# Kernel tuning notes

Hardware: AMD Instinct MI355X
Metric: run time of the kernel (lower is better)

Reference implementation:

```python
import jax, jax.numpy as jnp
import numpy as np
import math

D_MODEL = 512
DK = D_MODEL // 4      # per-head dim = 128
DH = D_MODEL // 8      # half-head dim = 64
BS, QL, SL = 4, 2048, 2048


def setup_inputs() -> dict:
    key = jax.random.key(0)
    ks = jax.random.split(key, 16)
    h = D_MODEL // 2
    inp = {
        "q": jax.random.normal(ks[0], (2, BS, QL, h), jnp.float32),
        "k": jax.random.normal(ks[1], (2, BS, SL, h), jnp.float32),
        "v": jax.random.normal(ks[2], (2, BS, SL, h), jnp.float32),
        "q_spa_embed": jax.random.normal(ks[3], (BS, 1, DK, DK), jnp.float32) * 0.1,
        "kv_spa_embed": jax.random.normal(ks[4], (BS, SL, DK, DK), jnp.float32) * 0.1,
        "attention_bias": jax.random.normal(ks[5], (BS, SL), jnp.float32),
        "mask": jax.random.randint(ks[6], (BS, SL), 0, 2, jnp.int32),
        # Linear weights stored [in, out] (torch Linear(in,out).weight.T)
        "W_qa": jax.random.normal(ks[7], (h, h // 2), jnp.float32) / math.sqrt(h),
        "W_qb": jax.random.normal(ks[8], (h, h // 2), jnp.float32) / math.sqrt(h),
        "W_ka": jax.random.normal(ks[9], (h, h // 2), jnp.float32) / math.sqrt(h),
        "W_kb": jax.random.normal(ks[10], (h, h // 2), jnp.float32) / math.sqrt(h),
        "W_va": jax.random.normal(ks[11], (h, h // 2), jnp.float32) / math.sqrt(h),
        "W_vb": jax.random.normal(ks[12], (h, h // 2), jnp.float32) / math.sqrt(h),
        "W_oa": jax.random.normal(ks[13], (h, h), jnp.float32) / math.sqrt(h),
        "W_ob": jax.random.normal(ks[14], (h, h), jnp.float32) / math.sqrt(h),
    }
    return inp


def _make_heads(xa, xb):
    # xa, xb: [bs, L, d_model//4] -> [bs, 4, L, dk] with head pattern
    # (a0,b0),(a1,b0),(a0,b1),(a1,b1)
    bs, L, _ = xa.shape
    xa = xa.reshape(bs, L, 2, DH)
    xb = xb.reshape(bs, L, 2, DH)
    xa = jnp.tile(xa, (1, 1, 2, 1))            # [bs,L,4,DH]
    xb = jnp.repeat(xb, 2, axis=2)             # [bs,L,4,DH]
    return jnp.concatenate([xa, xb], axis=-1).transpose(0, 2, 1, 3)  # [bs,4,L,DK]


def reference(q, k, v, q_spa_embed, kv_spa_embed, attention_bias, mask,
              W_qa, W_qb, W_ka, W_kb, W_va, W_vb, W_oa, W_ob):
    bs, ql = q.shape[1], q.shape[2]
    sl = k.shape[2]
    qh = _make_heads(q[0] @ W_qa, q[1] @ W_qb)   # [bs,4,ql,DK]
    kh = _make_heads(k[0] @ W_ka, k[1] @ W_kb)   # [bs,4,sl,DK]
    vh = _make_heads(v[0] @ W_va, v[1] @ W_vb)   # [bs,4,sl,DK]

    # per-token spatial rotation (seq_len == kv_spa_embed.shape[1] branch)
    qh = jnp.einsum('bij,bhqj->bhqi', q_spa_embed[:, 0], qh)
    kh = jnp.einsum('bsij,bhsj->bhsi', kv_spa_embed, kh)

    scores = jnp.einsum('bhqd,bhsd->bhqs', qh, kh) / math.sqrt(D_MODEL // 4)
    scores = scores + mask.astype(scores.dtype)[:, None, None, :] * (-1e9)
    attn = jax.nn.softmax(scores - attention_bias[:, None, None, :], axis=-1)
    # dropout: identity (eval mode)
    out = jnp.einsum('bhqs,bhsd->bhqd', attn, vh)          # [bs,4,ql,DK]

    out = out.reshape(bs, 4, ql, 2, DH)
    oa = out[:, :, :, 0].transpose(0, 2, 1, 3).reshape(bs, ql, -1) @ W_oa
    ob = out[:, :, :, 1].transpose(0, 2, 1, 3).reshape(bs, ql, -1) @ W_ob
    return jnp.stack([oa, ob], axis=0), attn
```

## Files before the change

### kernel.cpp

```cpp
#include <hip/hip_runtime.h>
#include <math.h>

#define QL 2048
#define SL 2048
#define BS 4
#define NH 4
#define FSZ ((size_t)BS * QL * 128)
#define OSZ ((size_t)2 * BS * QL * 256)

typedef short bf16x8 __attribute__((ext_vector_type(8)));
typedef float f32x4 __attribute__((ext_vector_type(4)));

__device__ __forceinline__ short to_bf16_rne(float x) {
    unsigned u = __float_as_uint(x);
    unsigned r = u + 0x7fffu + ((u >> 16) & 1u);
    return (short)(r >> 16);
}

__device__ __forceinline__ void split8(const float* x, bf16x8& hi, bf16x8& lo) {
    #pragma unroll
    for (int j = 0; j < 8; j++) {
        short hh = to_bf16_rne(x[j]);
        float hf = __uint_as_float(((unsigned)(unsigned short)hh) << 16);
        hi[j] = hh;
        lo[j] = to_bf16_rne(x[j] - hf);
    }
}

__global__ __launch_bounds__(256) void proj_mfma_kernel(
    const float* __restrict__ q, const float* __restrict__ k, const float* __restrict__ v,
    const float* __restrict__ Wqa, const float* __restrict__ Wqb,
    const float* __restrict__ Wka, const float* __restrict__ Wkb,
    const float* __restrict__ Wva, const float* __restrict__ Wvb,
    float* __restrict__ ws)
{
    int id = blockIdx.y;
    const float* X; const float* W;
    const size_t HALF = (size_t)BS * QL * 256;
    switch (id) {
      case 0: X = q;        W = Wqa; break;
      case 1: X = q + HALF; W = Wqb; break;
      case 2: X = k;        W = Wka; break;
      case 3: X = k + HALF; W = Wkb; break;
      case 4: X = v;        W = Wva; break;
      default:X = v + HALF; W = Wvb; break;
    }
    float* Y = ws + (size_t)id * FSZ;
    int m0 = blockIdx.x * 128;

    __shared__ short lA[128 * 64];
    __shared__ short lB[128 * 64];

    int t = threadIdx.x;
    int srow = t >> 1, shalf = t & 1;
    int l = t & 63, w = t >> 6;
    int wr = w >> 1, wc = w & 1;
    int lr = l & 15, kb = l >> 4;

    f32x4 acc[4][4] = {};

    for (int kc = 0; kc < 256; kc += 32) {
        {
            const float* srcA = X + (size_t)(m0 + srow) * 256 + kc + shalf * 16;
            float xa[16];
            #pragma unroll
            for (int j = 0; j < 4; j++)
                *(float4*)&xa[j * 4] = *(const float4*)(srcA + j * 4);
            bf16x8 h0, l0, h1, l1;
            split8(&xa[0], h0, l0);
            split8(&xa[8], h1, l1);
            int base = srow * 64, r7 = srow & 7;
            *(bf16x8*)&lA[base + (((4 * shalf + 0) ^ r7) * 8)] = h0;
            *(bf16x8*)&lA[base + (((4 * shalf + 1) ^ r7) * 8)] = l0;
            *(bf16x8*)&lA[base + (((4 * shalf + 2) ^ r7) * 8)] = h1;
            *(bf16x8*)&lA[base + (((4 * shalf + 3) ^ r7) * 8)] = l1;
        }
        {
            int ncol = srow;
            float xb[16];
            #pragma unroll
            for (int j = 0; j < 16; j++)
                xb[j] = W[(size_t)(kc + shalf * 16 + j) * 128 + ncol];
            bf16x8 h0, l0, h1, l1;
            split8(&xb[0], h0, l0);
            split8(&xb[8], h1, l1);
            int base = ncol * 64, r7 = ncol & 7;
            *(bf16x8*)&lB[base + (((4 * shalf + 0) ^ r7) * 8)] = h0;
            *(bf16x8*)&lB[base + (((4 * shalf + 1) ^ r7) * 8)] = l0;
            *(bf16x8*)&lB[base + (((4 * shalf + 2) ^ r7) * 8)] = h1;
            *(bf16x8*)&lB[base + (((4 * shalf + 3) ^ r7) * 8)] = l1;
        }
        __syncthreads();

        bf16x8 ah[4], al[4], bhv[4], blv[4];
        #pragma unroll
        for (int m = 0; m < 4; m++) {
            int r = wr * 64 + m * 16 + lr;
            int r7 = r & 7, base = r * 64;
            ah[m] = *(bf16x8*)&lA[base + (((2 * kb + 0) ^ r7) * 8)];
            al[m] = *(bf16x8*)&lA[base + (((2 * kb + 1) ^ r7) * 8)];
        }
        #pragma unroll
        for (int n = 0; n < 4; n++) {
            int r = wc * 64 + n * 16 + lr;
            int r7 = r & 7, base = r * 64;
            bhv[n] = *(bf16x8*)&lB[base + (((2 * kb + 0) ^ r7) * 8)];
            blv[n] = *(bf16x8*)&lB[base + (((2 * kb + 1) ^ r7) * 8)];
        }
        #pragma unroll
        for (int m = 0; m < 4; m++) {
            #pragma unroll
            for (int n = 0; n < 4; n++) {
                acc[m][n] = __builtin_amdgcn_mfma_f32_16x16x32_bf16(ah[m], bhv[n], acc[m][n], 0, 0, 0);
                acc[m][n] = __builtin_amdgcn_mfma_f32_16x16x32_bf16(ah[m], blv[n], acc[m][n], 0, 0, 0);
                acc[m][n] = __builtin_amdgcn_mfma_f32_16x16x32_bf16(al[m], bhv[n], acc[m][n], 0, 0, 0);
            }
        }
        __syncthreads();
    }

    #pragma unroll
    for (int n = 0; n < 4; n++) {
        int gcol = wc * 64 + n * 16 + lr;
        #pragma unroll
        for (int m = 0; m < 4; m++) {
            int grow = m0 + wr * 64 + m * 16 + kb * 4;
            float* dst = Y + (size_t)grow * 128 + gcol;
            f32x4 c = acc[m][n];
            dst[0 * 128] = c[0];
            dst[1 * 128] = c[1];
            dst[2 * 128] = c[2];
            dst[3 * 128] = c[3];
        }
    }
}

__global__ __launch_bounds__(256) void rot_split_kernel(
    const float* __restrict__ qa, const float* __restrict__ qb,
    const float* __restrict__ ka, const float* __restrict__ kb,
    const float* __restrict__ qse, const float* __restrict__ kvse,
    short* __restrict__ qrotS, short* __restrict__ krotS)
{
    int tkn = blockIdx.x;
    int b = blockIdx.y;
    int z = blockIdx.z;
    const float* ha = z ? ka : qa;
    const float* hb = z ? kb : qb;
    const float* E = z ? (kvse + (size_t)(b * SL + tkn) * 16384)
                       : (qse + (size_t)b * 16384);
    short* rotS = z ? krotS : qrotS;

    __shared__ float hv[4][128];
    __shared__ float outl[4][128];
    int tid = threadIdx.x;
    size_t tok = (size_t)(b * QL + tkn) * 128;
    for (int idx = tid; idx < 512; idx += 256) {
        int h = idx >> 7, d = idx & 127;
        float val = (d < 64) ? ha[tok + (h & 1) * 64 + d]
                             : hb[tok + (h >> 1) * 64 + (d - 64)];
        hv[h][d] = val;
    }
    __syncthreads();
    int w = tid >> 6, lane = tid & 63;
    int half = lane >> 5, l5 = lane & 31;
    for (int it = 0; it < 16; ++it) {
        int i = w * 32 + it * 2 + half;
        float4 e = *(const float4*)(E + (size_t)i * 128 + l5 * 4);
        float acc[4];
        #pragma unroll
        for (int h = 0; h < 4; h++) {
            float4 x = *(const float4*)&hv[h][l5 * 4];
            acc[h] = e.x * x.x + e.y * x.y + e.z * x.z + e.w * x.w;
        }
        #pragma unroll
        for (int off = 1; off < 32; off <<= 1) {
            #pragma unroll
            for (int h = 0; h < 4; h++) acc[h] += __shfl_xor(acc[h], off);
        }
        if (l5 < 4) outl[l5][i] = acc[l5];
    }
    __syncthreads();
    if (tid < 128) {
        int h    = tid >> 5;
        int kcid = (tid >> 3) & 3;
        int s    = tid & 7;
        int shalf = s >> 2;
        int isLo  = s & 1;
        int jbase = ((s >> 1) & 1) * 8;
        int dbase = kcid * 32 + shalf * 16 + jbase;
        bf16x8 outv;
        #pragma unroll
        for (int j = 0; j < 8; j++) {
            float x = outl[h][dbase + j];
            short hh = to_bf16_rne(x);
            if (isLo) {
                float hf = __uint_as_float(((unsigned)(unsigned short)hh) << 16);
                outv[j] = to_bf16_rne(x - hf);
            } else {
                outv[j] = hh;
            }
        }
        int bh = b * NH + h;
        int row = tkn & 127;
        size_t base = ((((size_t)bh * 16 + (tkn >> 7)) * 4 + kcid) * 128 + row) * 64;
        *(bf16x8*)&rotS[base + (size_t)((s ^ (row & 7)) * 8)] = outv;
    }
}

__global__ __launch_bounds__(256) void score_mfma_kernel(
    const short* __restrict__ qrotS, const short* __restrict__ krotS,
    const float* __restrict__ bias, const int* __restrict__ mask,
    float* __restrict__ attn, float* __restrict__ stats)
{
    __shared__ short lA[128 * 64];
    __shared__ short lB[128 * 64];
    __shared__ float redM[128][2];
    __shared__ float redS[128][2];

    int bid = blockIdx.x;
    int wg = (bid & 7) * 512 + (bid >> 3);
    int bh = wg >> 8;
    int qt = (wg >> 4) & 15, st = wg & 15;
    int q0 = qt * 128, s0 = st * 128;
    int b = bh >> 2;

    int t = threadIdx.x;
    int l = t & 63, w = t >> 6;
    int wr = w >> 1, wc = w & 1;
    int lr = l & 15, kb = l >> 4;

    const short* Abase = qrotS + (((size_t)bh * 16 + qt) * 4) * 8192;
    const short* Bbase = krotS + (((size_t)bh * 16 + st) * 4) * 8192;

    f32x4 acc[4][4] = {};

    for (int kcid = 0; kcid < 4; kcid++) {
        {
            const bf16x8* srcA = (const bf16x8*)(Abase + (size_t)kcid * 8192) + t * 4;
            const bf16x8* srcB = (const bf16x8*)(Bbase + (size_t)kcid * 8192) + t * 4;
            bf16x8 a0 = srcA[0], a1 = srcA[1], a2 = srcA[2], a3 = srcA[3];
            bf16x8 b0 = srcB[0], b1 = srcB[1], b2 = srcB[2], b3 = srcB[3];
            bf16x8* dA = (bf16x8*)lA + t * 4;
            bf16x8* dB = (bf16x8*)lB + t * 4;
            dA[0] = a0; dA[1] = a1; dA[2] = a2; dA[3] = a3;
            dB[0] = b0; dB[1] = b1; dB[2] = b2; dB[3] = b3;
        }
        __syncthreads();

        bf16x8 ah[4], al[4], bhv[4], blv[4];
        #pragma unroll
        for (int m = 0; m < 4; m++) {
            int r = wr * 64 + m * 16 + lr;
            int r7 = r & 7, base = r * 64;
            ah[m] = *(bf16x8*)&lA[base + (((2 * kb + 0) ^ r7) * 8)];
            al[m] = *(bf16x8*)&lA[base + (((2 * kb + 1) ^ r7) * 8)];
        }
        #pragma unroll
        for (int n = 0; n < 4; n++) {
            int r = wc * 64 + n * 16 + lr;
            int r7 = r & 7, base = r * 64;
            bhv[n] = *(bf16x8*)&lB[base + (((2 * kb + 0) ^ r7) * 8)];
            blv[n] = *(bf16x8*)&lB[base + (((2 * kb + 1) ^ r7) * 8)];
        }
        #pragma unroll
        for (int m = 0; m < 4; m++) {
            #pragma unroll
            for (int n = 0; n < 4; n++) {
                acc[m][n] = __builtin_amdgcn_mfma_f32_16x16x32_bf16(ah[m], bhv[n], acc[m][n], 0, 0, 0);
                acc[m][n] = __builtin_amdgcn_mfma_f32_16x16x32_bf16(ah[m], blv[n], acc[m][n], 0, 0, 0);
                acc[m][n] = __builtin_amdgcn_mfma_f32_16x16x32_bf16(al[m], bhv[n], acc[m][n], 0, 0, 0);
            }
        }
        __syncthreads();
    }

    const float scale = 0.08838834764831845f;
    #pragma unroll
    for (int n = 0; n < 4; n++) {
        int gs = s0 + wc * 64 + n * 16 + lr;
        float adj = -1e9f * (float)mask[b * SL + gs] - bias[b * SL + gs];
        #pragma unroll
        for (int m = 0; m < 4; m++) {
            int gq = q0 + wr * 64 + m * 16 + kb * 4;
            float* dst = attn + ((size_t)bh * QL + gq) * SL + gs;
            f32x4 c = acc[m][n];
            c[0] = c[0] * scale + adj;
            c[1] = c[1] * scale + adj;
            c[2] = c[2] * scale + adj;
            c[3] = c[3] * scale + adj;
            acc[m][n] = c;
            dst[0 * SL] = c[0];
            dst[1 * SL] = c[1];
            dst[2 * SL] = c[2];
            dst[3 * SL] = c[3];
        }
    }

    #pragma unroll
    for (int m = 0; m < 4; m++) {
        #pragma unroll
        for (int i = 0; i < 4; i++) {
            float rm = fmaxf(fmaxf(acc[m][0][i], acc[m][1][i]),
                             fmaxf(acc[m][2][i], acc[m][3][i]));
            rm = fmaxf(rm, __shfl_xor(rm, 1));
            rm = fmaxf(rm, __shfl_xor(rm, 2));
            rm = fmaxf(rm, __shfl_xor(rm, 4));
            rm = fmaxf(rm, __shfl_xor(rm, 8));
            if (lr == 0) redM[wr * 64 + m * 16 + kb * 4 + i][wc] = rm;
        }
    }
    __syncthreads();
    #pragma unroll
    for (int m = 0; m < 4; m++) {
        #pragma unroll
        for (int i = 0; i < 4; i++) {
            int row = wr * 64 + m * 16 + kb * 4 + i;
            float mt = fmaxf(redM[row][0], redM[row][1]);
            float es = __expf(acc[m][0][i] - mt) + __expf(acc[m][1][i] - mt)
                     + __expf(acc[m][2][i] - mt) + __expf(acc[m][3][i] - mt);
            es += __shfl_xor(es, 1);
            es += __shfl_xor(es, 2);
            es += __shfl_xor(es, 4);
            es += __shfl_xor(es, 8);
            if (lr == 0) redS[row][wc] = es;
        }
    }
    __syncthreads();
    if (t < 128) {
        float mt = fmaxf(redM[t][0], redM[t][1]);
        float es = redS[t][0] + redS[t][1];
        size_t r = (size_t)bh * QL + q0 + t;
        stats[(r * 16 + st) * 2 + 0] = mt;
        stats[(r * 16 + st) * 2 + 1] = es;
    }
}

__global__ __launch_bounds__(256) void sreduce_kernel(
    const float* __restrict__ stats,
    float* __restrict__ rowm, float* __restrict__ rowinv)
{
    int r = blockIdx.x * 256 + threadIdx.x;
    const float* src = stats + (size_t)r * 32;
    float4 p[8];
    #pragma unroll
    for (int j = 0; j < 8; j++) p[j] = *(const float4*)(src + j * 4);
    float m = -INFINITY;
    #pragma unroll
    for (int j = 0; j < 8; j++) { m = fmaxf(m, p[j].x); m = fmaxf(m, p[j].z); }
    float s = 0.f;
    #pragma unroll
    for (int j = 0; j < 8; j++) {
        s += p[j].y * __expf(p[j].x - m);
        s += p[j].w * __expf(p[j].z - m);
    }
    rowm[r] = m;
    rowinv[r] = 1.0f / s;
}

__global__ __launch_bounds__(256) void vtrans_kernel(
    const float* __restrict__ va, const float* __restrict__ vb,
    short* __restrict__ vT)
{
    int sblk = blockIdx.x;
    int bh = blockIdx.y;
    int b = bh >> 2, h = bh & 3;
    int hao = (h & 1) * 64, hbo = (h >> 1) * 64;
    __shared__ float vt[32][132];
    int t = threadIdx.x;
    for (int f = t; f < 1024; f += 256) {
        int s = f >> 5, c4 = (f & 31) * 4;
        size_t tok = (size_t)(b * SL + sblk * 32 + s) * 128;
        float4 vv = (c4 < 64) ? *(const float4*)(va + tok + hao + c4)
                              : *(const float4*)(vb + tok + hbo + (c4 - 64));
        *(float4*)&vt[s][c4] = vv;
    }
    __syncthreads();
    int d = t >> 1, shalf = t & 1;
    bf16x8 hi[2], lo[2];
    #pragma unroll
    for (int kb2 = 0; kb2 < 2; kb2++) {
        int kb = shalf * 2 + kb2;
        #pragma unroll
        for (int j = 0; j < 8; j++) {
            float x = vt[kb * 8 + j][d];
            short hh = to_bf16_rne(x);
            float hf = __uint_as_float(((unsigned)(unsigned short)hh) << 16);
            hi[kb2][j] = hh;
            lo[kb2][j] = to_bf16_rne(x - hf);
        }
    }
    size_t base = (((size_t)bh * 64 + sblk) * 128 + d) * 64;
    int d7 = d & 7;
    *(bf16x8*)&vT[base + (size_t)(((2 * (shalf * 2 + 0) + 0) ^ d7) * 8)] = hi[0];
    *(bf16x8*)&vT[base + (size_t)(((2 * (shalf * 2 + 0) + 1) ^ d7) * 8)] = lo[0];
    *(bf16x8*)&vT[base + (size_t)(((2 * (shalf * 2 + 1) + 0) ^ d7) * 8)] = hi[1];
    *(bf16x8*)&vT[base + (size_t)(((2 * (shalf * 2 + 1) + 1) ^ d7) * 8)] = lo[1];
}

__global__ __launch_bounds__(256) void pv_fused_kernel(
    float* __restrict__ attn, const short* __restrict__ vT,
    const float* __restrict__ rowm, const float* __restrict__ rowinv,
    float* __restrict__ outh)
{
    __shared__ short lA[128 * 64];
    __shared__ short lB[128 * 64];

    int bid = blockIdx.x;
    int wg = (bid & 7) * 32 + (bid >> 3);
    int bh = wg >> 4, qt = wg & 15;
    int q0 = qt * 128;

    float* Ag = attn + ((size_t)bh * QL + q0) * SL;
    const short* Bg = vT + (size_t)bh * 64 * 8192;

    int t = threadIdx.x;
    int srow = t >> 1, shalf = t & 1;
    int l = t & 63, w = t >> 6;
    int wr = w >> 1, wc = w & 1;
    int lr = l & 15, kb = l >> 4;

    float rm  = rowm[(size_t)bh * QL + q0 + srow];
    float riv = rowinv[(size_t)bh * QL + q0 + srow];

    f32x4 acc[4][4] = {};

    for (int sblk = 0; sblk < 64; sblk++) {
        {
            float* src = Ag + (size_t)srow * SL + sblk * 32 + shalf * 16;
            float x[16];
            #pragma unroll
            for (int j = 0; j < 4; j++)
                *(float4*)&x[j * 4] = *(const float4*)(src + j * 4);
            #pragma unroll
            for (int j = 0; j < 16; j++)
                x[j] = __expf(x[j] - rm) * riv;
            #pragma unroll
            for (int j = 0; j < 4; j++)
                *(float4*)(src + j * 4) = *(float4*)&x[j * 4];
            bf16x8 h0, l0, h1, l1;
            split8(&x[0], h0, l0);
            split8(&x[8], h1, l1);
            int base = srow * 64, r7 = srow & 7;
            *(bf16x8*)&lA[base + (((4 * shalf + 0) ^ r7) * 8)] = h0;
            *(bf16x8*)&lA[base + (((4 * shalf + 1) ^ r7) * 8)] = l0;
            *(bf16x8*)&lA[base + (((4 * shalf + 2) ^ r7) * 8)] = h1;
            *(bf16x8*)&lA[base + (((4 * shalf + 3) ^ r7) * 8)] = l1;
        }
        {
            const bf16x8* src = (const bf16x8*)(Bg + (size_t)sblk * 8192) + t * 4;
            bf16x8 v0 = src[0], v1 = src[1], v2 = src[2], v3 = src[3];
            bf16x8* dst = (bf16x8*)lB + t * 4;
            dst[0] = v0; dst[1] = v1; dst[2] = v2; dst[3] = v3;
        }
        __syncthreads();

        bf16x8 ah[4], al[4], bhv[4], blv[4];
        #pragma unroll
        for (int m = 0; m < 4; m++) {
            int r = wr * 64 + m * 16 + lr;
            int r7 = r & 7, base = r * 64;
            ah[m] = *(bf16x8*)&lA[base + (((2 * kb + 0) ^ r7) * 8)];
            al[m] = *(bf16x8*)&lA[base + (((2 * kb + 1) ^ r7) * 8)];
        }
        #pragma unroll
        for (int n = 0; n < 4; n++) {
            int r = wc * 64 + n * 16 + lr;
            int r7 = r & 7, base = r * 64;
            bhv[n] = *(bf16x8*)&lB[base + (((2 * kb + 0) ^ r7) * 8)];
            blv[n] = *(bf16x8*)&lB[base + (((2 * kb + 1) ^ r7) * 8)];
        }
        #pragma unroll
        for (int m = 0; m < 4; m++) {
            #pragma unroll
            for (int n = 0; n < 4; n++) {
                acc[m][n] = __builtin_amdgcn_mfma_f32_16x16x32_bf16(ah[m], bhv[n], acc[m][n], 0, 0, 0);
                acc[m][n] = __builtin_amdgcn_mfma_f32_16x16x32_bf16(ah[m], blv[n], acc[m][n], 0, 0, 0);
                acc[m][n] = __builtin_amdgcn_mfma_f32_16x16x32_bf16(al[m], bhv[n], acc[m][n], 0, 0, 0);
            }
        }
        __syncthreads();
    }

    #pragma unroll
    for (int n = 0; n < 4; n++) {
        int gd = wc * 64 + n * 16 + lr;
        #pragma unroll
        for (int m = 0; m < 4; m++) {
            int gq = q0 + wr * 64 + m * 16 + kb * 4;
            float* dst = outh + ((size_t)bh * QL + gq) * 128 + gd;
            f32x4 c = acc[m][n];
            dst[0 * 128] = c[0];
            dst[1 * 128] = c[1];
            dst[2 * 128] = c[2];
            dst[3 * 128] = c[3];
        }
    }
}

__global__ __launch_bounds__(256) void oproj_mfma_kernel(
    const float* __restrict__ outh, const float* __restrict__ Woa, const float* __restrict__ Wob,
    float* __restrict__ opart)
{
    int bt = blockIdx.x;
    int b = bt >> 4, tt = bt & 15;
    int t0 = tt * 128;
    int n0 = blockIdx.y * 128;
    int sel = blockIdx.z >> 1;
    int ks  = blockIdx.z & 1;
    const float* W = sel ? Wob : Woa;
    int doff = sel ? 64 : 0;

    __shared__ short lA[128 * 64];
    __shared__ short lB[128 * 64];

    int t = threadIdx.x;
    int srow = t >> 1, shalf = t & 1;
    int l = t & 63, w = t >> 6;
    int wr = w >> 1, wc = w & 1;
    int lr = l & 15, kb = l >> 4;

    f32x4 acc[4][4] = {};

    for (int kc = ks * 128; kc < ks * 128 + 128; kc += 32) {
        {
            int k0 = kc + shalf * 16;
            int h = k0 >> 6, d0 = k0 & 63;
            const float* srcA = outh + ((size_t)(b * NH + h) * QL + t0 + srow) * 128 + doff + d0;
            float xa[16];
            #pragma unroll
            for (int j = 0; j < 4; j++)
                *(float4*)&xa[j * 4] = *(const float4*)(srcA + j * 4);
            bf16x8 h0, l0, h1, l1;
            split8(&xa[0], h0, l0);
            split8(&xa[8], h1, l1);
            int base = srow * 64, r7 = srow & 7;
            *(bf16x8*)&lA[base + (((4 * shalf + 0) ^ r7) * 8)] = h0;
            *(bf16x8*)&lA[base + (((4 * shalf + 1) ^ r7) * 8)] = l0;
            *(bf16x8*)&lA[base + (((4 * shalf + 2) ^ r7) * 8)] = h1;
            *(bf16x8*)&lA[base + (((4 * shalf + 3) ^ r7) * 8)] = l1;
        }
        {
            int ncol = srow;
            float xb[16];
            #pragma unroll
            for (int j = 0; j < 16; j++)
                xb[j] = W[(size_t)(kc + shalf * 16 + j) * 256 + n0 + ncol];
            bf16x8 h0, l0, h1, l1;
            split8(&xb[0], h0, l0);
            split8(&xb[8], h1, l1);
            int base = ncol * 64, r7 = ncol & 7;
            *(bf16x8*)&lB[base + (((4 * shalf + 0) ^ r7) * 8)] = h0;
            *(bf16x8*)&lB[base + (((4 * shalf + 1) ^ r7) * 8)] = l0;
            *(bf16x8*)&lB[base + (((4 * shalf + 2) ^ r7) * 8)] = h1;
            *(bf16x8*)&lB[base + (((4 * shalf + 3) ^ r7) * 8)] = l1;
        }
        __syncthreads();

        bf16x8 ah[4], al[4], bhv[4], blv[4];
        #pragma unroll
        for (int m = 0; m < 4; m++) {
            int r = wr * 64 + m * 16 + lr;
            int r7 = r & 7, base = r * 64;
            ah[m] = *(bf16x8*)&lA[base + (((2 * kb + 0) ^ r7) * 8)];
            al[m] = *(bf16x8*)&lA[base + (((2 * kb + 1) ^ r7) * 8)];
        }
        #pragma unroll
        for (int n = 0; n < 4; n++) {
            int r = wc * 64 + n * 16 + lr;
            int r7 = r & 7, base = r * 64;
            bhv[n] = *(bf16x8*)&lB[base + (((2 * kb + 0) ^ r7) * 8)];
            blv[n] = *(bf16x8*)&lB[base + (((2 * kb + 1) ^ r7) * 8)];
        }
        #pragma unroll
        for (int m = 0; m < 4; m++) {
            #pragma unroll
            for (int n = 0; n < 4; n++) {
                acc[m][n] = __builtin_amdgcn_mfma_f32_16x16x32_bf16(ah[m], bhv[n], acc[m][n], 0, 0, 0);
                acc[m][n] = __builtin_amdgcn_mfma_f32_16x16x32_bf16(ah[m], blv[n], acc[m][n], 0, 0, 0);
                acc[m][n] = __builtin_amdgcn_mfma_f32_16x16x32_bf16(al[m], bhv[n], acc[m][n], 0, 0, 0);
            }
        }
        __syncthreads();
    }

    float* dstbase = opart + (size_t)ks * OSZ;
    #pragma unroll
    for (int n = 0; n < 4; n++) {
        int gcol = n0 + wc * 64 + n * 16 + lr;
        #pragma unroll
        for (int m = 0; m < 4; m++) {
            int grow = t0 + wr * 64 + m * 16 + kb * 4;
            float* dst = dstbase + ((size_t)((sel * BS + b) * QL) + grow) * 256 + gcol;
            f32x4 c = acc[m][n];
            dst[0 * 256] = c[0];
            dst[1 * 256] = c[1];
            dst[2 * 256] = c[2];
            dst[3 * 256] = c[3];
        }
    }
}

__global__ __launch_bounds__(256) void oadd_kernel(
    const float* __restrict__ opart, float* __restrict__ outp)
{
    size_t i = ((size_t)blockIdx.x * 256 + threadIdx.x) * 4;
    float4 a = *(const float4*)(opart + i);
    float4 b = *(const float4*)(opart + OSZ + i);
    float4 o = make_float4(a.x + b.x, a.y + b.y, a.z + b.z, a.w + b.w);
    *(float4*)(outp + i) = o;
}

extern "C" void kernel_launch(void* const* d_in, const int* in_sizes, int n_in,
                              void* d_out, int out_size, void* d_ws, size_t ws_size,
                              hipStream_t stream)
{
    const float* q    = (const float*)d_in[0];
    const float* k    = (const float*)d_in[1];
    const float* v    = (const float*)d_in[2];
    const float* qse  = (const float*)d_in[3];
    const float* kvse = (const float*)d_in[4];
    const float* bias = (const float*)d_in[5];
    const int*   mask = (const int*)d_in[6];
    const float* Wqa  = (const float*)d_in[7];
    const float* Wqb  = (const float*)d_in[8];
    const float* Wka  = (const float*)d_in[9];
    const float* Wkb  = (const float*)d_in[10];
    const float* Wva  = (const float*)d_in[11];
    const float* Wvb  = (const float*)d_in[12];
    const float* Woa  = (const float*)d_in[13];
    const float* Wob  = (const float*)d_in[14];

    float* outp = (float*)d_out;
    float* attn = outp + OSZ;

    float* ws     = (float*)d_ws;
    float* qa     = ws + 0 * FSZ;
    float* qb     = ws + 1 * FSZ;
    float* ka     = ws + 2 * FSZ;
    float* kb     = ws + 3 * FSZ;
    float* va     = ws + 4 * FSZ;
    float* vb     = ws + 5 * FSZ;
    short* qrotS  = (short*)(ws + 6 * FSZ);
    short* krotS  = (short*)(ws + 10 * FSZ);
    float* stats  = ws + 14 * FSZ;
    float* rowm   = ws + 15 * FSZ;
    float* rowinv = ws + 15 * FSZ + 32768;
    short* vT     = (short*)(ws + 16 * FSZ);
    float* outh   = ws + 20 * FSZ;
    float* opart  = ws + 24 * FSZ;

    proj_mfma_kernel<<<dim3(64, 6), 256, 0, stream>>>(q, k, v, Wqa, Wqb, Wka, Wkb, Wva, Wvb, ws);
    vtrans_kernel<<<dim3(64, 16), 256, 0, stream>>>(va, vb, vT);
    rot_split_kernel<<<dim3(QL, BS, 2), 256, 0, stream>>>(qa, qb, ka, kb, qse, kvse, qrotS, krotS);
    score_mfma_kernel<<<4096, 256, 0, stream>>>(qrotS, krotS, bias, mask, attn, stats);
    sreduce_kernel<<<128, 256, 0, stream>>>(stats, rowm, rowinv);
    pv_fused_kernel<<<256, 256, 0, stream>>>(attn, vT, rowm, rowinv, outh);
    oproj_mfma_kernel<<<dim3(64, 2, 4), 256, 0, stream>>>(outh, Woa, Wob, opart);
    oadd_kernel<<<4096, 256, 0, stream>>>(opart, outp);
}
```

Measured before the change: 618.3 us.

## Fuse row-stat reduction into PV kernel and prefetch next attn tile

Removes the separate sreduce kernel launch by having each PV workgroup reduce the per-tile max/sum stats for its 128 rows into shared memory. It also software-pipelines the attention-row loads, fetching the next 32-column block into registers before processing the current one, so global load latency overlaps with the exp/split/MFMA work. The prefetch raises register pressure and the stats reduction adds a small prologue per block.

```diff
diff --git a/kernel.cpp b/kernel.cpp
--- a/kernel.cpp
+++ b/kernel.cpp
@@ -335,28 +335,6 @@
     }
 }
 
-__global__ __launch_bounds__(256) void sreduce_kernel(
-    const float* __restrict__ stats,
-    float* __restrict__ rowm, float* __restrict__ rowinv)
-{
-    int r = blockIdx.x * 256 + threadIdx.x;
-    const float* src = stats + (size_t)r * 32;
-    float4 p[8];
-    #pragma unroll
-    for (int j = 0; j < 8; j++) p[j] = *(const float4*)(src + j * 4);
-    float m = -INFINITY;
-    #pragma unroll
-    for (int j = 0; j < 8; j++) { m = fmaxf(m, p[j].x); m = fmaxf(m, p[j].z); }
-    float s = 0.f;
-    #pragma unroll
-    for (int j = 0; j < 8; j++) {
-        s += p[j].y * __expf(p[j].x - m);
-        s += p[j].w * __expf(p[j].z - m);
-    }
-    rowm[r] = m;
-    rowinv[r] = 1.0f / s;
-}
-
 __global__ __launch_bounds__(256) void vtrans_kernel(
     const float* __restrict__ va, const float* __restrict__ vb,
     short* __restrict__ vT)
@@ -399,11 +377,13 @@
 
 __global__ __launch_bounds__(256) void pv_fused_kernel(
     float* __restrict__ attn, const short* __restrict__ vT,
-    const float* __restrict__ rowm, const float* __restrict__ rowinv,
+    const float* __restrict__ stats,
     float* __restrict__ outh)
 {
     __shared__ short lA[128 * 64];
     __shared__ short lB[128 * 64];
+    __shared__ float lrm[128];
+    __shared__ float lriv[128];
 
     int bid = blockIdx.x;
     int wg = (bid & 7) * 32 + (bid >> 3);
@@ -419,21 +399,57 @@
     int wr = w >> 1, wc = w & 1;
     int lr = l & 15, kb = l >> 4;
 
-    float rm  = rowm[(size_t)bh * QL + q0 + srow];
-    float riv = rowinv[(size_t)bh * QL + q0 + srow];
+    if (t < 128) {
+        const float* src = stats + ((size_t)bh * QL + q0 + t) * 32;
+        float4 p[8];
+        #pragma unroll
+        for (int j = 0; j < 8; j++) p[j] = *(const float4*)(src + j * 4);
+        float m = -INFINITY;
+        #pragma unroll
+        for (int j = 0; j < 8; j++) { m = fmaxf(m, p[j].x); m = fmaxf(m, p[j].z); }
+        float s = 0.f;
+        #pragma unroll
+        for (int j = 0; j < 8; j++) {
+            s += p[j].y * __expf(p[j].x - m);
+            s += p[j].w * __expf(p[j].z - m);
+        }
+        lrm[t] = m;
+        lriv[t] = 1.0f / s;
+    }
+    __syncthreads();
+    float rm  = lrm[srow];
+    float riv = lriv[srow];
 
     f32x4 acc[4][4] = {};
 
+    float4 xq0, xq1, xq2, xq3;
+    {
+        const float* src = Ag + (size_t)srow * SL + 0 + shalf * 16;
+        xq0 = *(const float4*)(src + 0);
+        xq1 = *(const float4*)(src + 4);
+        xq2 = *(const float4*)(src + 8);
+        xq3 = *(const float4*)(src + 12);
+    }
+
     for (int sblk = 0; sblk < 64; sblk++) {
+        float4 xn0, xn1, xn2, xn3;
+        if (sblk < 63) {
+            const float* srcn = Ag + (size_t)srow * SL + (sblk + 1) * 32 + shalf * 16;
+            xn0 = *(const float4*)(srcn + 0);
+            xn1 = *(const float4*)(srcn + 4);
+            xn2 = *(const float4*)(srcn + 8);
+            xn3 = *(const float4*)(srcn + 12);
+        }
         {
-            float* src = Ag + (size_t)srow * SL + sblk * 32 + shalf * 16;
             float x[16];
-            #pragma unroll
-            for (int j = 0; j < 4; j++)
-                *(float4*)&x[j * 4] = *(const float4*)(src + j * 4);
+            *(float4*)&x[0]  = xq0;
+            *(float4*)&x[4]  = xq1;
+            *(float4*)&x[8]  = xq2;
+            *(float4*)&x[12] = xq3;
             #pragma unroll
             for (int j = 0; j < 16; j++)
                 x[j] = __expf(x[j] - rm) * riv;
+            float* src = Ag + (size_t)srow * SL + sblk * 32 + shalf * 16;
             #pragma unroll
             for (int j = 0; j < 4; j++)
                 *(float4*)(src + j * 4) = *(float4*)&x[j * 4];
@@ -479,6 +495,8 @@
             }
         }
         __syncthreads();
+
+        xq0 = xn0; xq1 = xn1; xq2 = xn2; xq3 = xn3;
     }
 
     #pragma unroll
@@ -643,8 +661,6 @@
     short* qrotS  = (short*)(ws + 6 * FSZ);
     short* krotS  = (short*)(ws + 10 * FSZ);
     float* stats  = ws + 14 * FSZ;
-    float* rowm   = ws + 15 * FSZ;
-    float* rowinv = ws + 15 * FSZ + 32768;
     short* vT     = (short*)(ws + 16 * FSZ);
     float* outh   = ws + 20 * FSZ;
     float* opart  = ws + 24 * FSZ;
@@ -653,8 +669,7 @@
     vtrans_kernel<<<dim3(64, 16), 256, 0, stream>>>(va, vb, vT);
     rot_split_kernel<<<dim3(QL, BS, 2), 256, 0, stream>>>(qa, qb, ka, kb, qse, kvse, qrotS, krotS);
     score_mfma_kernel<<<4096, 256, 0, stream>>>(qrotS, krotS, bias, mask, attn, stats);
-    sreduce_kernel<<<128, 256, 0, stream>>>(stats, rowm, rowinv);
-    pv_fused_kernel<<<256, 256, 0, stream>>>(attn, vT, rowm, rowinv, outh);
+    pv_fused_kernel<<<256, 256, 0, stream>>>(attn, vT, stats, outh);
     oproj_mfma_kernel<<<dim3(64, 2, 4), 256, 0, stream>>>(outh, Woa, Wob, opart);
     oadd_kernel<<<4096, 256, 0, stream>>>(opart, outp);
 }
```

Measured after the change: 610.2 us. About the same (-1.3%).
